# Kernel tuning notes

Hardware: AMD Instinct MI355X
Metric: run time of the kernel (lower is better)

Reference implementation:

```python
import jax, jax.numpy as jnp
import numpy as np

B, T, F_IN, L, D = 512, 32, 4096, 256, 256
EPS = 1e-8
KM_ITERS = 100


def _linear(x, w, b):
    return x @ w.T + b


def _clf(h, w0, b0, w1, b1, w2, b2, w3, b3):
    # Linear->ReLU (Dropout is identity in eval) x3 then final Linear
    h = jax.nn.relu(_linear(h, w0, b0))
    h = jax.nn.relu(_linear(h, w1, b1))
    h = jax.nn.relu(_linear(h, w2, b2))
    return _linear(h, w3, b3)


def _kmeans_cosine(f):
    # f: (T, L). 2-cluster kmeans with cosine distance, fixed iteration count.
    fn = f / (jnp.linalg.norm(f, axis=1, keepdims=True) + EPS)
    centers0 = jnp.stack([f[0], f[T // 2]])  # deterministic init (ref: random pick)

    def step(centers, _):
        cn = centers / (jnp.linalg.norm(centers, axis=1, keepdims=True) + EPS)
        sim = fn @ cn.T                           # (T,2) cosine similarity
        assign = jnp.argmax(sim, axis=1)          # argmin of (1 - sim)
        mask = jax.nn.one_hot(assign, 2, dtype=f.dtype)  # (T,2)
        counts = mask.sum(axis=0)                 # (2,)
        new = (mask.T @ f) / jnp.clip(counts, 1.0)[:, None]
        new = jnp.where(counts[:, None] > 0, new, centers)
        return new, assign

    centers, assigns = jax.lax.scan(step, centers0, None, length=KM_ITERS)
    return assigns[-1], centers


def setup_inputs() -> dict:
    key = jax.random.key(0)
    ks = jax.random.split(key, 32)
    s = 0.02
    inp = {
        "x": jax.random.normal(ks[0], (B, T, F_IN), dtype=jnp.float32),
        "tsn_w": jax.random.normal(ks[1], (L, F_IN, 3), dtype=jnp.float32) * s,
        "tsn_b": jnp.zeros((L,), jnp.float32),
        "aV_w": jax.random.normal(ks[2], (D, L), dtype=jnp.float32) * s,
        "aV_b": jnp.zeros((D,), jnp.float32),
        "aU_w": jax.random.normal(ks[3], (D, L), dtype=jnp.float32) * s,
        "aU_b": jnp.zeros((D,), jnp.float32),
        "gate_w": jax.random.normal(ks[4], (1, D), dtype=jnp.float32) * s,
        "gate_b": jnp.zeros((1,), jnp.float32),
    }
    dims_bag = [(D, L), (D // 2, D), (32, D // 2), (1, 32)]
    dims_seg = [(D, L + 1), (D // 2, D), (32, D // 2), (1, 32)]
    for j, (o, i) in enumerate(dims_bag):
        inp[f"cb_w{j}"] = jax.random.normal(ks[5 + j], (o, i), dtype=jnp.float32) * s
        inp[f"cb_b{j}"] = jnp.zeros((o,), jnp.float32)
    for j, (o, i) in enumerate(dims_seg):
        inp[f"cs_w{j}"] = jax.random.normal(ks[9 + j], (o, i), dtype=jnp.float32) * s
        inp[f"cs_b{j}"] = jnp.zeros((o,), jnp.float32)
    return inp


def reference(x, tsn_w, tsn_b, aV_w, aV_b, aU_w, aU_b, gate_w, gate_b,
              cb_w0, cb_b0, cb_w1, cb_b1, cb_w2, cb_b2, cb_w3, cb_b3,
              cs_w0, cs_b0, cs_w1, cs_b1, cs_w2, cs_b2, cs_w3, cs_b3):
    feat_in = jnp.nan_to_num(x)  # (B,T,4096)
    # Conv1d over time (kernel 3, pad 1): NCH layout
    feature = jax.lax.conv_general_dilated(
        feat_in.transpose(0, 2, 1), tsn_w, (1,), [(1, 1)],
        dimension_numbers=('NCH', 'OIH', 'NCH')) + tsn_b[None, :, None]
    feature = feature.transpose(0, 2, 1)  # (B,T,L)

    # Gated MIL attention
    A_V = jnp.tanh(_linear(feature, aV_w, aV_b))
    A_U = jax.nn.sigmoid(_linear(feature, aU_w, aU_b))
    A = _linear(A_V * A_U, gate_w, gate_b)      # (B,T,1)
    At = A.transpose(0, 2, 1)                   # (B,1,T)
    bag = jnp.einsum('bot,btl->bol', jax.nn.softmax(At, axis=2), feature)[:, 0]  # (B,L)

    output1 = jax.nn.sigmoid(_clf(bag, cb_w0, cb_b0, cb_w1, cb_b1,
                                  cb_w2, cb_b2, cb_w3, cb_b3)).reshape(-1)  # (B,)

    seg_in = jnp.concatenate([feature, A], axis=2)  # (B,T,L+1)
    output_seg = jax.nn.sigmoid(_clf(seg_in, cs_w0, cs_b0, cs_w1, cs_b1,
                                     cs_w2, cs_b2, cs_w3, cs_b3)[..., 0])  # (B,T)

    # Per-sample 2-means cosine clustering (batched via vmap instead of python loop)
    assigns, _ = jax.vmap(_kmeans_cosine)(feature)  # (B,T) int
    mask0 = assigns == 0
    cnt0 = mask0.sum(1).astype(output_seg.dtype)
    cnt1 = T - cnt0
    m0 = jnp.where(mask0, output_seg, 0.0).sum(1) / jnp.clip(cnt0, 1.0)
    m1 = jnp.where(~mask0, output_seg, 0.0).sum(1) / jnp.clip(cnt1, 1.0)
    m0 = jnp.where(cnt0 > 0, m0, -jnp.inf)
    m1 = jnp.where(cnt1 > 0, m1, -jnp.inf)
    output2 = jnp.maximum(m0, m1)  # (B,)

    weight = 0.5
    output = jnp.stack([output1 * weight, output2 * (1.0 - weight)], axis=1)  # (B,2)
    # (ragged cluster index lists replaced by the dense assignment map `assigns`)
    return feature, assigns, output_seg, output, At
```

## Files before the change

### kernel.cpp

```cpp
#include <hip/hip_runtime.h>
#include <cfloat>
#include <cmath>

#define NB 512
#define NT 32
#define FIN 4096
#define NL 256
#define ND 256
#define NM (NB*NT)
#define KCONV (3*FIN)
#define PLANE 3145728

#define BM 128
#define BN 128
#define BK 32
#define LDT 132

typedef __attribute__((ext_vector_type(8))) short short8_t;
typedef __attribute__((ext_vector_type(4))) float f32x4;

__device__ __forceinline__ float sigmoidf_(float v) { return 1.0f / (1.0f + expf(-v)); }

__device__ __forceinline__ unsigned short f2bf(float v) {
  unsigned u = __float_as_uint(v);
  unsigned r = u + 0x7FFFu + ((u >> 16) & 1u);
  return (unsigned short)(r >> 16);
}
__device__ __forceinline__ float bf2f(unsigned short h) {
  return __uint_as_float(((unsigned)h) << 16);
}

__global__ void __launch_bounds__(256) repack_frag_k(const float* __restrict__ w,
                                                     unsigned short* __restrict__ wt) {
  int d = blockIdx.x * 256 + threadIdx.x;
  int kt = d >> 13;
  int bc = (d >> 9) & 15;
  int lane = (d >> 3) & 63;
  int j = d & 7;
  int kb = lane >> 4;
  int kk = kt * 32 + kb * 8 + j;
  int l = bc * 16 + (lane & 15);
  int tap = kk >> 12;
  int f = kk & 4095;
  float v = w[(size_t)l * KCONV + f * 3 + tap];
  unsigned short hi = f2bf(v);
  unsigned short lo = f2bf(v - bf2f(hi));
  wt[d] = hi;
  wt[PLANE + d] = lo;
}

__global__ void __launch_bounds__(256) repack_dense_k(const float* __restrict__ W1,
    const float* __restrict__ W2, int nsplit, int ldw, int KB, int N16,
    unsigned short* __restrict__ wt, int planeElems) {
  int d = blockIdx.x * 256 + threadIdx.x;
  if (d >= planeElems) return;
  int j = d & 7;
  int lane = (d >> 3) & 63;
  int bckt = d >> 9;
  int bc = bckt % N16;
  int kt = bckt / N16;
  int kk = kt * 32 + (lane >> 4) * 8 + j;
  int l = bc * 16 + (lane & 15);
  float v = 0.f;
  if (kk < KB) {
    if (l < nsplit) v = W1[(size_t)l * ldw + kk];
    else            v = W2[(size_t)(l - nsplit) * ldw + kk];
  }
  unsigned short hi = f2bf(v);
  unsigned short lo = f2bf(v - bf2f(hi));
  wt[d] = hi;
  wt[planeElems + d] = lo;
}

__global__ void __launch_bounds__(256) conv_mfma_k(const float* __restrict__ x,
    const unsigned short* __restrict__ WT, float* __restrict__ PART) {
  __shared__ __align__(16) unsigned short AS[8192];
  __shared__ __align__(16) unsigned short BS[8192];
  const int tid = threadIdx.x;
  const int m0 = blockIdx.x * 128;
  const int by = blockIdx.y;
  const int ktBase = blockIdx.z * 192;
  const int lane = tid & 63;
  const int w = tid >> 6, wr = w >> 1, wc = w & 1;
  const int kb = tid & 3;
  const int rquot = tid >> 2;

  f32x4 acc[4][4] = {};
  float4 avreg[4];
  short8_t bvreg[4];

  {
    int ktg = ktBase;
    int tap = ktg >> 7;
    int f0 = (ktg & 127) << 5;
#pragma unroll
    for (int u = 0; u < 2; ++u) {
      int row = u * 64 + rquot;
      int gm = m0 + row;
      int tt = (gm & 31) + tap - 1;
      if ((unsigned)tt < 32u) {
        const float* src = x + (size_t)(gm + tap - 1) * FIN + f0 + kb * 8;
        avreg[u*2+0] = *reinterpret_cast<const float4*>(src);
        avreg[u*2+1] = *reinterpret_cast<const float4*>(src + 4);
      } else {
        avreg[u*2+0] = make_float4(0,0,0,0);
        avreg[u*2+1] = make_float4(0,0,0,0);
      }
    }
    const unsigned short* bsrc = WT + ((size_t)ktg * 16 + by * 8) * 512;
#pragma unroll
    for (int q = 0; q < 4; ++q) {
      int p = q >> 1, pass = q & 1;
      bvreg[q] = *reinterpret_cast<const short8_t*>(bsrc + (size_t)p * PLANE + (pass*256 + tid) * 8);
    }
  }

  for (int i = 0; i < 192; ++i) {
#pragma unroll
    for (int u = 0; u < 2; ++u) {
      float vv[8];
      *reinterpret_cast<float4*>(&vv[0]) = avreg[u*2+0];
      *reinterpret_cast<float4*>(&vv[4]) = avreg[u*2+1];
      __align__(16) unsigned short hi[8];
      __align__(16) unsigned short lo[8];
#pragma unroll
      for (int e = 0; e < 8; ++e) {
        float v = vv[e];
        v = (v == v) ? v : 0.0f;
        unsigned short h = f2bf(v);
        hi[e] = h;
        lo[e] = f2bf(v - bf2f(h));
      }
      int row = u * 64 + rquot;
      int br = row >> 4;
      int lanew = (row & 15) + (kb << 4);
      int off = br * 512 + lanew * 8;
      *reinterpret_cast<short8_t*>(AS + off)        = *reinterpret_cast<const short8_t*>(hi);
      *reinterpret_cast<short8_t*>(AS + 4096 + off) = *reinterpret_cast<const short8_t*>(lo);
    }
#pragma unroll
    for (int q = 0; q < 4; ++q) {
      int p = q >> 1, pass = q & 1;
      *reinterpret_cast<short8_t*>(BS + p * 4096 + (pass*256 + tid) * 8) = bvreg[q];
    }
    __syncthreads();

    if (i + 1 < 192) {
      int ktg = ktBase + i + 1;
      int tap = ktg >> 7;
      int f0 = (ktg & 127) << 5;
#pragma unroll
      for (int u = 0; u < 2; ++u) {
        int row = u * 64 + rquot;
        int gm = m0 + row;
        int tt = (gm & 31) + tap - 1;
        if ((unsigned)tt < 32u) {
          const float* src = x + (size_t)(gm + tap - 1) * FIN + f0 + kb * 8;
          avreg[u*2+0] = *reinterpret_cast<const float4*>(src);
          avreg[u*2+1] = *reinterpret_cast<const float4*>(src + 4);
        } else {
          avreg[u*2+0] = make_float4(0,0,0,0);
          avreg[u*2+1] = make_float4(0,0,0,0);
        }
      }
      const unsigned short* bsrc = WT + ((size_t)ktg * 16 + by * 8) * 512;
#pragma unroll
      for (int q = 0; q < 4; ++q) {
        int p = q >> 1, pass = q & 1;
        bvreg[q] = *reinterpret_cast<const short8_t*>(bsrc + (size_t)p * PLANE + (pass*256 + tid) * 8);
      }
    }

    short8_t bh[4], bl[4];
#pragma unroll
    for (int c = 0; c < 4; ++c) {
      int bc = wc * 4 + c;
      bh[c] = *reinterpret_cast<const short8_t*>(BS + bc * 512 + lane * 8);
      bl[c] = *reinterpret_cast<const short8_t*>(BS + 4096 + bc * 512 + lane * 8);
    }
#pragma unroll
    for (int r = 0; r < 4; ++r) {
      int br = wr * 4 + r;
      short8_t ah = *reinterpret_cast<const short8_t*>(AS + br * 512 + lane * 8);
      short8_t al = *reinterpret_cast<const short8_t*>(AS + 4096 + br * 512 + lane * 8);
#pragma unroll
      for (int c = 0; c < 4; ++c) {
        acc[r][c] = __builtin_amdgcn_mfma_f32_16x16x32_bf16(ah, bh[c], acc[r][c], 0, 0, 0);
        acc[r][c] = __builtin_amdgcn_mfma_f32_16x16x32_bf16(ah, bl[c], acc[r][c], 0, 0, 0);
        acc[r][c] = __builtin_amdgcn_mfma_f32_16x16x32_bf16(al, bh[c], acc[r][c], 0, 0, 0);
      }
    }
    __syncthreads();
  }

  float* P = PART + (size_t)blockIdx.z * ((size_t)NM * NL);
#pragma unroll
  for (int r = 0; r < 4; ++r) {
#pragma unroll
    for (int c = 0; c < 4; ++c) {
#pragma unroll
      for (int e = 0; e < 4; ++e) {
        int row = m0 + wr * 64 + r * 16 + ((lane >> 4) << 2) + e;
        int col = by * 128 + wc * 64 + c * 16 + (lane & 15);
        P[(size_t)row * NL + col] = acc[r][c][e];
      }
    }
  }
}

__global__ void __launch_bounds__(256) reduce_bias_k(const float* __restrict__ PART,
    const float* __restrict__ bias, float* __restrict__ feat) {
  int i = blockIdx.x * 256 + threadIdx.x;
  size_t base = (size_t)i * 4;
  float4 a = *reinterpret_cast<const float4*>(PART + base);
  float4 b = *reinterpret_cast<const float4*>(PART + (size_t)NM * NL + base);
  int c0 = (int)(base & 255);
  float4 bb = *reinterpret_cast<const float4*>(bias + c0);
  float4 o;
  o.x = a.x + b.x + bb.x;
  o.y = a.y + b.y + bb.y;
  o.z = a.z + b.z + bb.z;
  o.w = a.w + b.w + bb.w;
  *reinterpret_cast<float4*>(feat + base) = o;
}

template <int ACT, int SEG>
__global__ void __launch_bounds__(256) mfma_gemm_k(const float* __restrict__ A, int lda,
    const float* __restrict__ Aws, const unsigned short* __restrict__ WT,
    int planeElems, int N16, int KT,
    const float* __restrict__ bias1, const float* __restrict__ bias2, int bsplit,
    float* __restrict__ C, int N) {
  __shared__ __align__(16) unsigned short AS[8192];
  __shared__ __align__(16) unsigned short BS[8192];
  const int tid = threadIdx.x;
  const int m0 = blockIdx.x * 128;
  const int by = blockIdx.y;
  const int lane = tid & 63;
  const int w = tid >> 6, wr = w >> 1, wc = w & 1;
  const int kb = tid & 3;
  const int rquot = tid >> 2;

  f32x4 acc[4][4] = {};
  float4 avreg[4];
  short8_t bvreg[4];

  {
    int kk0 = 0;
#pragma unroll
    for (int u = 0; u < 2; ++u) {
      int gm = m0 + u * 64 + rquot;
      const float* src = A + (size_t)gm * lda + kk0 + kb * 8;
      avreg[u*2+0] = *reinterpret_cast<const float4*>(src);
      avreg[u*2+1] = *reinterpret_cast<const float4*>(src + 4);
    }
    const unsigned short* bsrc = WT + ((size_t)(0 * N16) + by * 8) * 512;
#pragma unroll
    for (int q = 0; q < 4; ++q) {
      int p = q >> 1, pass = q & 1;
      bvreg[q] = *reinterpret_cast<const short8_t*>(bsrc + (size_t)p * planeElems * 8 / 8
                  + (size_t)p * 0 + (pass*256 + tid) * 8 + (size_t)(p ? planeElems - planeElems : 0));
    }
#pragma unroll
    for (int q = 0; q < 4; ++q) {
      int p = q >> 1, pass = q & 1;
      bvreg[q] = *reinterpret_cast<const short8_t*>(WT + (size_t)p * planeElems
                  + ((size_t)by * 8) * 512 + (pass*256 + tid) * 8);
    }
  }

  for (int i = 0; i < KT; ++i) {
#pragma unroll
    for (int u = 0; u < 2; ++u) {
      float vv[8];
      *reinterpret_cast<float4*>(&vv[0]) = avreg[u*2+0];
      *reinterpret_cast<float4*>(&vv[4]) = avreg[u*2+1];
      __align__(16) unsigned short hi[8];
      __align__(16) unsigned short lo[8];
#pragma unroll
      for (int e = 0; e < 8; ++e) {
        float v = vv[e];
        unsigned short h = f2bf(v);
        hi[e] = h;
        lo[e] = f2bf(v - bf2f(h));
      }
      int row = u * 64 + rquot;
      int br = row >> 4;
      int lanew = (row & 15) + (kb << 4);
      int off = br * 512 + lanew * 8;
      *reinterpret_cast<short8_t*>(AS + off)        = *reinterpret_cast<const short8_t*>(hi);
      *reinterpret_cast<short8_t*>(AS + 4096 + off) = *reinterpret_cast<const short8_t*>(lo);
    }
#pragma unroll
    for (int q = 0; q < 4; ++q) {
      int p = q >> 1, pass = q & 1;
      *reinterpret_cast<short8_t*>(BS + p * 4096 + (pass*256 + tid) * 8) = bvreg[q];
    }
    __syncthreads();

    if (i + 1 < KT) {
      int kk0 = (i + 1) * 32;
#pragma unroll
      for (int u = 0; u < 2; ++u) {
        int gm = m0 + u * 64 + rquot;
        if (SEG && kk0 >= 256) {
          float a0 = (kb == 0) ? Aws[gm] : 0.f;
          avreg[u*2+0] = make_float4(a0, 0.f, 0.f, 0.f);
          avreg[u*2+1] = make_float4(0.f, 0.f, 0.f, 0.f);
        } else {
          const float* src = A + (size_t)gm * lda + kk0 + kb * 8;
          avreg[u*2+0] = *reinterpret_cast<const float4*>(src);
          avreg[u*2+1] = *reinterpret_cast<const float4*>(src + 4);
        }
      }
#pragma unroll
      for (int q = 0; q < 4; ++q) {
        int p = q >> 1, pass = q & 1;
        bvreg[q] = *reinterpret_cast<const short8_t*>(WT + (size_t)p * planeElems
                    + ((size_t)(i + 1) * N16 + by * 8) * 512 + (pass*256 + tid) * 8);
      }
    }

    short8_t bh[4], bl[4];
#pragma unroll
    for (int c = 0; c < 4; ++c) {
      int bc = wc * 4 + c;
      bh[c] = *reinterpret_cast<const short8_t*>(BS + bc * 512 + lane * 8);
      bl[c] = *reinterpret_cast<const short8_t*>(BS + 4096 + bc * 512 + lane * 8);
    }
#pragma unroll
    for (int r = 0; r < 4; ++r) {
      int br = wr * 4 + r;
      short8_t ah = *reinterpret_cast<const short8_t*>(AS + br * 512 + lane * 8);
      short8_t al = *reinterpret_cast<const short8_t*>(AS + 4096 + br * 512 + lane * 8);
#pragma unroll
      for (int c = 0; c < 4; ++c) {
        acc[r][c] = __builtin_amdgcn_mfma_f32_16x16x32_bf16(ah, bh[c], acc[r][c], 0, 0, 0);
        acc[r][c] = __builtin_amdgcn_mfma_f32_16x16x32_bf16(ah, bl[c], acc[r][c], 0, 0, 0);
        acc[r][c] = __builtin_amdgcn_mfma_f32_16x16x32_bf16(al, bh[c], acc[r][c], 0, 0, 0);
      }
    }
    __syncthreads();
  }

#pragma unroll
  for (int r = 0; r < 4; ++r) {
#pragma unroll
    for (int c = 0; c < 4; ++c) {
#pragma unroll
      for (int e = 0; e < 4; ++e) {
        int row = m0 + wr * 64 + r * 16 + ((lane >> 4) << 2) + e;
        int col = by * 128 + wc * 64 + c * 16 + (lane & 15);
        float b = (col < bsplit) ? bias1[col] : bias2[col - bsplit];
        float v = acc[r][c][e] + b;
        if (ACT == 1) v = fmaxf(v, 0.f);
        C[(size_t)row * N + col] = v;
      }
    }
  }
}

template <int ACT>
__global__ void __launch_bounds__(256) gemm_wt_k(const float* __restrict__ A, int lda,
    const float* __restrict__ W, int ldw, int KB,
    const float* __restrict__ bias, float* __restrict__ C,
    int N, int K) {
  __shared__ float As[BK][LDT];
  __shared__ float Bs[BK][LDT];
  const int tid = threadIdx.x;
  const int m0 = blockIdx.x * BM;
  const int n0 = blockIdx.y * BN;
  const int row0 = (tid >> 4) << 3;
  const int col0 = (tid & 15) << 3;
  float acc[8][8] = {};
  for (int kk0 = 0; kk0 < K; kk0 += BK) {
#pragma unroll
    for (int i = 0; i < 4; ++i) {
      int v = i * 256 + tid;
      int row = v >> 3;
      int f4 = (v & 7) << 2;
      float4 val = *reinterpret_cast<const float4*>(A + (size_t)(m0 + row) * lda + kk0 + f4);
      As[f4 + 0][row] = val.x;
      As[f4 + 1][row] = val.y;
      As[f4 + 2][row] = val.z;
      As[f4 + 3][row] = val.w;
    }
#pragma unroll
    for (int i = 0; i < 4; ++i) {
      int v = i * 256 + tid;
      int n = v >> 3;
      int kq = (v & 7) << 2;
      int gn = n0 + n;
#pragma unroll
      for (int j = 0; j < 4; ++j) {
        int kk = kk0 + kq + j;
        float bv = 0.f;
        if (gn < N && kk < KB) bv = W[(size_t)gn * ldw + kk];
        Bs[kq + j][n] = bv;
      }
    }
    __syncthreads();
#pragma unroll
    for (int kk = 0; kk < BK; ++kk) {
      float a[8], b[8];
      *reinterpret_cast<float4*>(&a[0]) = *reinterpret_cast<const float4*>(&As[kk][row0]);
      *reinterpret_cast<float4*>(&a[4]) = *reinterpret_cast<const float4*>(&As[kk][row0 + 4]);
      *reinterpret_cast<float4*>(&b[0]) = *reinterpret_cast<const float4*>(&Bs[kk][col0]);
      *reinterpret_cast<float4*>(&b[4]) = *reinterpret_cast<const float4*>(&Bs[kk][col0 + 4]);
#pragma unroll
      for (int r = 0; r < 8; ++r)
#pragma unroll
        for (int c = 0; c < 8; ++c)
          acc[r][c] = fmaf(a[r], b[c], acc[r][c]);
    }
    __syncthreads();
  }
#pragma unroll
  for (int r = 0; r < 8; ++r) {
    int m = m0 + row0 + r;
#pragma unroll
    for (int c = 0; c < 8; ++c) {
      int n = n0 + col0 + c;
      if (n < N) {
        float v = acc[r][c] + bias[n];
        if (ACT == 1) v = fmaxf(v, 0.f);
        C[(size_t)m * (size_t)N + n] = v;
      }
    }
  }
}

__global__ void __launch_bounds__(256) gate_k(const float* __restrict__ Y,
    const float* __restrict__ gw, const float* __restrict__ gb,
    float* __restrict__ Aws, float* __restrict__ At) {
  int lane = threadIdx.x & 63;
  int m = blockIdx.x * 4 + (threadIdx.x >> 6);
  float4 v4 = *reinterpret_cast<const float4*>(Y + (size_t)m * 512 + lane * 4);
  float4 u4 = *reinterpret_cast<const float4*>(Y + (size_t)m * 512 + 256 + lane * 4);
  float4 g4 = *reinterpret_cast<const float4*>(gw + lane * 4);
  float s = tanhf(v4.x) * sigmoidf_(u4.x) * g4.x
          + tanhf(v4.y) * sigmoidf_(u4.y) * g4.y
          + tanhf(v4.z) * sigmoidf_(u4.z) * g4.z
          + tanhf(v4.w) * sigmoidf_(u4.w) * g4.w;
#pragma unroll
  for (int off = 32; off > 0; off >>= 1) s += __shfl_xor(s, off, 64);
  if (lane == 0) {
    float a = s + gb[0];
    Aws[m] = a;
    At[m] = a;
  }
}

__global__ void __launch_bounds__(256) softmax_bag_k(const float* __restrict__ Aws,
    const float* __restrict__ feat, float* __restrict__ bag) {
  __shared__ float av[NT];
  __shared__ float ev[NT];
  int b = blockIdx.x, tid = threadIdx.x;
  if (tid < NT) av[tid] = Aws[b * NT + tid];
  __syncthreads();
  float mx = -FLT_MAX;
#pragma unroll
  for (int t = 0; t < NT; ++t) mx = fmaxf(mx, av[t]);
  if (tid < NT) ev[tid] = expf(av[tid] - mx);
  __syncthreads();
  float ssum = 0.f;
#pragma unroll
  for (int t = 0; t < NT; ++t) ssum += ev[t];
  float accv = 0.f;
#pragma unroll
  for (int t = 0; t < NT; ++t) accv += ev[t] * feat[((size_t)b * NT + t) * NL + tid];
  bag[(size_t)b * NL + tid] = accv / ssum;
}

__global__ void __launch_bounds__(256) rowdot32_k(const float* __restrict__ H,
    const float* __restrict__ w, const float* __restrict__ bptr,
    float* __restrict__ outp, int ostride, float scale) {
  int m = blockIdx.x * 256 + threadIdx.x;
  const float* h = H + (size_t)m * 32;
  float s = bptr[0];
#pragma unroll
  for (int i = 0; i < 32; i += 4) {
    float4 hv = *reinterpret_cast<const float4*>(h + i);
    float4 wv = *reinterpret_cast<const float4*>(w + i);
    s += hv.x * wv.x + hv.y * wv.y + hv.z * wv.z + hv.w * wv.w;
  }
  outp[(size_t)m * ostride] = scale * sigmoidf_(s);
}

__global__ void __launch_bounds__(64) kmeans_k(const float* __restrict__ feat,
    const float* __restrict__ seg, float* __restrict__ assigns_out,
    float* __restrict__ outpair) {
  __shared__ float fls[NT][260];
  int b = blockIdx.x, lane = threadIdx.x;
  int l0 = lane << 2;
  float fn[NT][4];
#pragma unroll
  for (int t = 0; t < NT; ++t) {
    float4 v = *reinterpret_cast<const float4*>(feat + ((size_t)b * NT + t) * NL + l0);
    *reinterpret_cast<float4*>(&fls[t][l0]) = v;
    float ss = v.x * v.x + v.y * v.y + v.z * v.z + v.w * v.w;
#pragma unroll
    for (int off = 32; off > 0; off >>= 1) ss += __shfl_xor(ss, off, 64);
    float nr = sqrtf(ss) + 1e-8f;
    fn[t][0] = v.x / nr; fn[t][1] = v.y / nr; fn[t][2] = v.z / nr; fn[t][3] = v.w / nr;
  }
  __syncthreads();
  float cr0[4], cr1[4];
#pragma unroll
  for (int i = 0; i < 4; ++i) { cr0[i] = fls[0][l0 + i]; cr1[i] = fls[16][l0 + i]; }

  unsigned long long amask = 0ull;
  unsigned long long prev = ~0ull;
  int c1n = 0;
  for (int it = 0; it < 100; ++it) {
    float ss0 = cr0[0]*cr0[0] + cr0[1]*cr0[1] + cr0[2]*cr0[2] + cr0[3]*cr0[3];
    float ss1 = cr1[0]*cr1[0] + cr1[1]*cr1[1] + cr1[2]*cr1[2] + cr1[3]*cr1[3];
#pragma unroll
    for (int off = 32; off > 0; off >>= 1) {
      ss0 += __shfl_xor(ss0, off, 64);
      ss1 += __shfl_xor(ss1, off, 64);
    }
    float nr0 = sqrtf(ss0) + 1e-8f, nr1 = sqrtf(ss1) + 1e-8f;
    float cn0[4], cn1[4];
#pragma unroll
    for (int i = 0; i < 4; ++i) { cn0[i] = cr0[i] / nr0; cn1[i] = cr1[i] / nr1; }
    float p[64];
#pragma unroll
    for (int t = 0; t < NT; ++t) {
      p[2*t]   = fn[t][0]*cn0[0] + fn[t][1]*cn0[1] + fn[t][2]*cn0[2] + fn[t][3]*cn0[3];
      p[2*t+1] = fn[t][0]*cn1[0] + fn[t][1]*cn1[1] + fn[t][2]*cn1[2] + fn[t][3]*cn1[3];
    }
    float v32[32];
    { bool hi = (lane & 32) != 0;
#pragma unroll
      for (int i = 0; i < 32; ++i) {
        float keep = hi ? p[32+i] : p[i];
        float send = hi ? p[i] : p[32+i];
        v32[i] = keep + __shfl_xor(send, 32, 64);
      } }
    float v16[16];
    { bool hi = (lane & 16) != 0;
#pragma unroll
      for (int i = 0; i < 16; ++i) {
        float keep = hi ? v32[16+i] : v32[i];
        float send = hi ? v32[i] : v32[16+i];
        v16[i] = keep + __shfl_xor(send, 16, 64);
      } }
    float v8[8];
    { bool hi = (lane & 8) != 0;
#pragma unroll
      for (int i = 0; i < 8; ++i) {
        float keep = hi ? v16[8+i] : v16[i];
        float send = hi ? v16[i] : v16[8+i];
        v8[i] = keep + __shfl_xor(send, 8, 64);
      } }
    float v4[4];
    { bool hi = (lane & 4) != 0;
#pragma unroll
      for (int i = 0; i < 4; ++i) {
        float keep = hi ? v8[4+i] : v8[i];
        float send = hi ? v8[i] : v8[4+i];
        v4[i] = keep + __shfl_xor(send, 4, 64);
      } }
    float v2[2];
    { bool hi = (lane & 2) != 0;
#pragma unroll
      for (int i = 0; i < 2; ++i) {
        float keep = hi ? v4[2+i] : v4[i];
        float send = hi ? v4[i] : v4[2+i];
        v2[i] = keep + __shfl_xor(send, 2, 64);
      } }
    float sim;
    { bool hi = (lane & 1) != 0;
      float keep = hi ? v2[1] : v2[0];
      float send = hi ? v2[0] : v2[1];
      sim = keep + __shfl_xor(send, 1, 64);
    }
    float simo = __shfl_xor(sim, 1, 64);
    bool is0 = (lane & 1) == 0;
    unsigned long long mask = __ballot(is0 && (simo > sim));
    int c1 = __popcll(mask);
    int c0 = NT - c1;
    amask = mask; c1n = c1;
    if (mask == prev) break;
    prev = mask;
    float s0v[4] = {0,0,0,0}, s1v[4] = {0,0,0,0};
#pragma unroll
    for (int t = 0; t < NT; ++t) {
      float mt = (float)((mask >> (2*t)) & 1ull);
      float nt = 1.0f - mt;
      float4 fv = *reinterpret_cast<const float4*>(&fls[t][l0]);
      s1v[0] = fmaf(mt, fv.x, s1v[0]); s1v[1] = fmaf(mt, fv.y, s1v[1]);
      s1v[2] = fmaf(mt, fv.z, s1v[2]); s1v[3] = fmaf(mt, fv.w, s1v[3]);
      s0v[0] = fmaf(nt, fv.x, s0v[0]); s0v[1] = fmaf(nt, fv.y, s0v[1]);
      s0v[2] = fmaf(nt, fv.z, s0v[2]); s0v[3] = fmaf(nt, fv.w, s0v[3]);
    }
    float fc0 = fmaxf((float)c0, 1.0f), fc1 = fmaxf((float)c1, 1.0f);
#pragma unroll
    for (int i = 0; i < 4; ++i) {
      float n0v = s0v[i] / fc0;
      float n1v = s1v[i] / fc1;
      cr0[i] = (c0 > 0) ? n0v : cr0[i];
      cr1[i] = (c1 > 0) ? n1v : cr1[i];
    }
  }
  if (lane < NT)
    assigns_out[(size_t)b * NT + lane] = (amask & (1ull << (2*lane))) ? 1.0f : 0.0f;
  if (lane == 0) {
    float sum0 = 0.f, sum1 = 0.f;
    for (int t = 0; t < NT; ++t) {
      float sv = seg[(size_t)b * NT + t];
      if (amask & (1ull << (2*t))) sum1 += sv; else sum0 += sv;
    }
    int c1 = c1n, c0 = NT - c1n;
    float m0 = (c0 > 0) ? (sum0 / fmaxf((float)c0, 1.f)) : -INFINITY;
    float m1 = (c1 > 0) ? (sum1 / fmaxf((float)c1, 1.f)) : -INFINITY;
    outpair[(size_t)b * 2 + 1] = 0.5f * fmaxf(m0, m1);
  }
}

extern "C" void kernel_launch(void* const* d_in, const int* in_sizes, int n_in,
                              void* d_out, int out_size, void* d_ws, size_t ws_size,
                              hipStream_t stream) {
  const float* x      = (const float*)d_in[0];
  const float* tsn_w  = (const float*)d_in[1];
  const float* tsn_b  = (const float*)d_in[2];
  const float* aV_w   = (const float*)d_in[3];
  const float* aV_b   = (const float*)d_in[4];
  const float* aU_w   = (const float*)d_in[5];
  const float* aU_b   = (const float*)d_in[6];
  const float* gate_w = (const float*)d_in[7];
  const float* gate_b = (const float*)d_in[8];
  const float* cb_w0  = (const float*)d_in[9];
  const float* cb_b0  = (const float*)d_in[10];
  const float* cb_w1  = (const float*)d_in[11];
  const float* cb_b1  = (const float*)d_in[12];
  const float* cb_w2  = (const float*)d_in[13];
  const float* cb_b2  = (const float*)d_in[14];
  const float* cb_w3  = (const float*)d_in[15];
  const float* cb_b3  = (const float*)d_in[16];
  const float* cs_w0  = (const float*)d_in[17];
  const float* cs_b0  = (const float*)d_in[18];
  const float* cs_w1  = (const float*)d_in[19];
  const float* cs_b1  = (const float*)d_in[20];
  const float* cs_w2  = (const float*)d_in[21];
  const float* cs_b2  = (const float*)d_in[22];
  const float* cs_w3  = (const float*)d_in[23];
  const float* cs_b3  = (const float*)d_in[24];

  float* out = (float*)d_out;
  float* o_feat   = out;
  float* o_assign = out + 4194304;
  float* o_seg    = out + 4210688;
  float* o_out    = out + 4227072;
  float* o_At     = out + 4228096;

  char* ws = (char*)d_ws;
  unsigned short* WT = (unsigned short*)ws;
  float* PART  = (float*)(ws + 12582912);
  unsigned short* WVU = (unsigned short*)ws;
  unsigned short* WC0 = (unsigned short*)(ws + 524288);
  unsigned short* WC1 = (unsigned short*)(ws + 819200);
  float* AWS   = (float*)(ws + 950272);
  float* BAG   = (float*)(ws + 1015808);
  float* BH0   = (float*)(ws + 1540096);
  float* BH1   = (float*)(ws + 2064384);
  float* BH2   = (float*)(ws + 2326528);
  float* Y     = (float*)(ws + 12582912);
  float* SH0   = (float*)(ws + 12582912);
  float* SH1   = (float*)(ws + 29360128);
  float* SH2   = (float*)(ws + 37748736);

  repack_frag_k<<<dim3(12288), dim3(256), 0, stream>>>(tsn_w, WT);
  conv_mfma_k<<<dim3(128, 2, 2), dim3(256), 0, stream>>>(x, WT, PART);
  reduce_bias_k<<<dim3(4096), dim3(256), 0, stream>>>(PART, tsn_b, o_feat);
  repack_dense_k<<<dim3(512), dim3(256), 0, stream>>>(aV_w, aU_w, 256, 256, 256, 32, WVU, 131072);
  repack_dense_k<<<dim3(288), dim3(256), 0, stream>>>(cs_w0, cs_w0, 256, 257, 257, 16, WC0, 73728);
  repack_dense_k<<<dim3(128), dim3(256), 0, stream>>>(cs_w1, cs_w1, 256, 256, 256, 8, WC1, 32768);
  mfma_gemm_k<0,0><<<dim3(128, 4), dim3(256), 0, stream>>>(o_feat, 256, nullptr, WVU,
      131072, 32, 8, aV_b, aU_b, 256, Y, 512);
  gate_k<<<dim3(4096), dim3(256), 0, stream>>>(Y, gate_w, gate_b, AWS, o_At);
  softmax_bag_k<<<dim3(512), dim3(256), 0, stream>>>(AWS, o_feat, BAG);
  gemm_wt_k<1><<<dim3(4, 2), dim3(256), 0, stream>>>(BAG, 256, cb_w0, 256, 256, cb_b0, BH0, 256, 256);
  gemm_wt_k<1><<<dim3(4, 1), dim3(256), 0, stream>>>(BH0, 256, cb_w1, 256, 256, cb_b1, BH1, 128, 256);
  gemm_wt_k<1><<<dim3(4, 1), dim3(256), 0, stream>>>(BH1, 128, cb_w2, 128, 128, cb_b2, BH2, 32, 128);
  rowdot32_k<<<dim3(2), dim3(256), 0, stream>>>(BH2, cb_w3, cb_b3, o_out, 2, 0.5f);
  mfma_gemm_k<1,1><<<dim3(128, 2), dim3(256), 0, stream>>>(o_feat, 256, AWS, WC0,
      73728, 16, 9, cs_b0, cs_b0, 256, SH0, 256);
  mfma_gemm_k<1,0><<<dim3(128, 1), dim3(256), 0, stream>>>(SH0, 256, nullptr, WC1,
      32768, 8, 8, cs_b1, cs_b1, 128, SH1, 128);
  gemm_wt_k<1><<<dim3(128, 1), dim3(256), 0, stream>>>(SH1, 128, cs_w2, 128, 128, cs_b2, SH2, 32, 128);
  rowdot32_k<<<dim3(64), dim3(256), 0, stream>>>(SH2, cs_w3, cs_b3, o_seg, 1, 1.0f);
  kmeans_k<<<dim3(512), dim3(64), 0, stream>>>(o_feat, o_seg, o_assign, o_out);
}
```

Before: 625.6 us.

## Pre-split input to bf16 hi/lo planes and stream conv tiles via async LDS loads

```diff
diff --git a/kernel.cpp b/kernel.cpp
--- a/kernel.cpp
+++ b/kernel.cpp
@@ -10,6 +10,7 @@
 #define NM (NB*NT)
 #define KCONV (3*FIN)
 #define PLANE 3145728
+#define KTILES 192
 
 #define BM 128
 #define BN 128
@@ -28,6 +29,33 @@
 }
 __device__ __forceinline__ float bf2f(unsigned short h) {
   return __uint_as_float(((unsigned)h) << 16);
+}
+
+__global__ void __launch_bounds__(256) xprep_k(const float* __restrict__ x,
+    unsigned short* __restrict__ XPhi, unsigned short* __restrict__ XPlo,
+    unsigned short* __restrict__ ZROW) {
+  size_t i = ((size_t)blockIdx.x * 256 + threadIdx.x) * 8;
+  float4 v0 = *reinterpret_cast<const float4*>(x + i);
+  float4 v1 = *reinterpret_cast<const float4*>(x + i + 4);
+  float vv[8];
+  *reinterpret_cast<float4*>(&vv[0]) = v0;
+  *reinterpret_cast<float4*>(&vv[4]) = v1;
+  __align__(16) unsigned short hi[8];
+  __align__(16) unsigned short lo[8];
+#pragma unroll
+  for (int e = 0; e < 8; ++e) {
+    float v = vv[e];
+    v = (v == v) ? v : 0.0f;
+    unsigned short h = f2bf(v);
+    hi[e] = h;
+    lo[e] = f2bf(v - bf2f(h));
+  }
+  *reinterpret_cast<short8_t*>(XPhi + i) = *reinterpret_cast<const short8_t*>(hi);
+  *reinterpret_cast<short8_t*>(XPlo + i) = *reinterpret_cast<const short8_t*>(lo);
+  if (blockIdx.x == 0 && threadIdx.x < 64) {
+    short8_t z = {0,0,0,0,0,0,0,0};
+    *reinterpret_cast<short8_t*>(ZROW + threadIdx.x * 8) = z;
+  }
 }
 
 __global__ void __launch_bounds__(256) repack_frag_k(const float* __restrict__ w,
@@ -72,6 +100,115 @@
   wt[planeElems + d] = lo;
 }
 
+__global__ void __launch_bounds__(256) conv_mfma2_k(
+    const unsigned short* __restrict__ XPhi, const unsigned short* __restrict__ XPlo,
+    const unsigned short* __restrict__ WT, const unsigned short* __restrict__ ZROW,
+    float* __restrict__ PART) {
+  __shared__ __align__(16) unsigned short LB[2][16384];
+  const int tid = threadIdx.x;
+  const int lane = tid & 63;
+  const int w = tid >> 6;
+  const int wr = w >> 1, wc = w & 1;
+  const int m0 = blockIdx.x * 128;
+  const int by = blockIdx.y;
+  const int ktBase = blockIdx.z * KTILES;
+  const int arow_lo = lane & 15;
+  const int achunk = lane >> 4;
+
+  f32x4 acc[4][4] = {};
+
+  auto stage = [&](int buf, int kt) {
+    const int tap = kt >> 7;
+    const int f0 = (kt & 127) << 5;
+#pragma unroll
+    for (int rb = 0; rb < 2; ++rb) {
+      const int br = (w << 1) + rb;
+      const int gm = m0 + br * 16 + arow_lo;
+      const int tt = (gm & 31) + tap - 1;
+      const unsigned short* sh;
+      const unsigned short* sl;
+      if ((unsigned)tt < 32u) {
+        const size_t off = (size_t)(gm + tap - 1) * 4096 + (size_t)(f0 + (achunk << 3));
+        sh = XPhi + off;
+        sl = XPlo + off;
+      } else {
+        sh = ZROW + (lane << 3);
+        sl = sh;
+      }
+      __builtin_amdgcn_global_load_lds(
+          (const __attribute__((address_space(1))) void*)sh,
+          (__attribute__((address_space(3))) void*)&LB[buf][br << 9], 16, 0, 0);
+      __builtin_amdgcn_global_load_lds(
+          (const __attribute__((address_space(1))) void*)sl,
+          (__attribute__((address_space(3))) void*)&LB[buf][4096 + (br << 9)], 16, 0, 0);
+    }
+#pragma unroll
+    for (int cb = 0; cb < 2; ++cb) {
+      const int bc = (w << 1) + cb;
+      const unsigned short* sh = WT + (((size_t)kt * 16 + (by << 3) + bc) << 9) + (lane << 3);
+      const unsigned short* sl = sh + PLANE;
+      __builtin_amdgcn_global_load_lds(
+          (const __attribute__((address_space(1))) void*)sh,
+          (__attribute__((address_space(3))) void*)&LB[buf][8192 + (bc << 9)], 16, 0, 0);
+      __builtin_amdgcn_global_load_lds(
+          (const __attribute__((address_space(1))) void*)sl,
+          (__attribute__((address_space(3))) void*)&LB[buf][12288 + (bc << 9)], 16, 0, 0);
+    }
+  };
+
+  stage(0, ktBase);
+  for (int i = 0; i < KTILES; ++i) {
+    const int cur = i & 1;
+    if (i + 1 < KTILES) {
+      stage(cur ^ 1, ktBase + i + 1);
+      asm volatile("s_waitcnt vmcnt(8)" ::: "memory");
+    } else {
+      asm volatile("s_waitcnt vmcnt(0)" ::: "memory");
+    }
+    __builtin_amdgcn_sched_barrier(0);
+    __builtin_amdgcn_s_barrier();
+
+    const unsigned short* A0 = &LB[cur][0];
+    const unsigned short* B0 = &LB[cur][8192];
+    short8_t bh[4], bl[4];
+#pragma unroll
+    for (int c = 0; c < 4; ++c) {
+      const int bc = wc * 4 + c;
+      bh[c] = *reinterpret_cast<const short8_t*>(B0 + (bc << 9) + (lane << 3));
+      bl[c] = *reinterpret_cast<const short8_t*>(B0 + 4096 + (bc << 9) + (lane << 3));
+    }
+#pragma unroll
+    for (int r = 0; r < 4; ++r) {
+      const int br = wr * 4 + r;
+      short8_t ah = *reinterpret_cast<const short8_t*>(A0 + (br << 9) + (lane << 3));
+      short8_t al = *reinterpret_cast<const short8_t*>(A0 + 4096 + (br << 9) + (lane << 3));
+#pragma unroll
+      for (int c = 0; c < 4; ++c) {
+        acc[r][c] = __builtin_amdgcn_mfma_f32_16x16x32_bf16(ah, bh[c], acc[r][c], 0, 0, 0);
+        acc[r][c] = __builtin_amdgcn_mfma_f32_16x16x32_bf16(ah, bl[c], acc[r][c], 0, 0, 0);
+        acc[r][c] = __builtin_amdgcn_mfma_f32_16x16x32_bf16(al, bh[c], acc[r][c], 0, 0, 0);
+      }
+    }
+    __builtin_amdgcn_sched_barrier(0);
+    asm volatile("s_waitcnt lgkmcnt(0)" ::: "memory");
+    __builtin_amdgcn_s_barrier();
+  }
+
+  float* P = PART + (size_t)blockIdx.z * ((size_t)NM * NL);
+#pragma unroll
+  for (int r = 0; r < 4; ++r) {
+#pragma unroll
+    for (int c = 0; c < 4; ++c) {
+#pragma unroll
+      for (int e = 0; e < 4; ++e) {
+        int row = m0 + wr * 64 + r * 16 + ((lane >> 4) << 2) + e;
+        int col = by * 128 + wc * 64 + c * 16 + (lane & 15);
+        P[(size_t)row * NL + col] = acc[r][c][e];
+      }
+    }
+  }
+}
+
 __global__ void __launch_bounds__(256) conv_mfma_k(const float* __restrict__ x,
     const unsigned short* __restrict__ WT, float* __restrict__ PART) {
   __shared__ __align__(16) unsigned short AS[8192];
@@ -245,20 +382,12 @@
   short8_t bvreg[4];
 
   {
-    int kk0 = 0;
 #pragma unroll
     for (int u = 0; u < 2; ++u) {
       int gm = m0 + u * 64 + rquot;
-      const float* src = A + (size_t)gm * lda + kk0 + kb * 8;
+      const float* src = A + (size_t)gm * lda + kb * 8;
       avreg[u*2+0] = *reinterpret_cast<const float4*>(src);
       avreg[u*2+1] = *reinterpret_cast<const float4*>(src + 4);
-    }
-    const unsigned short* bsrc = WT + ((size_t)(0 * N16) + by * 8) * 512;
-#pragma unroll
-    for (int q = 0; q < 4; ++q) {
-      int p = q >> 1, pass = q & 1;
-      bvreg[q] = *reinterpret_cast<const short8_t*>(bsrc + (size_t)p * planeElems * 8 / 8
-                  + (size_t)p * 0 + (pass*256 + tid) * 8 + (size_t)(p ? planeElems - planeElems : 0));
     }
 #pragma unroll
     for (int q = 0; q < 4; ++q) {
@@ -669,9 +798,18 @@
   float* SH0   = (float*)(ws + 12582912);
   float* SH1   = (float*)(ws + 29360128);
   float* SH2   = (float*)(ws + 37748736);
+  unsigned short* XPhi = (unsigned short*)(ws + 50331648);
+  unsigned short* XPlo = (unsigned short*)(ws + 184549376);
+  unsigned short* ZROW = (unsigned short*)(ws + 318767104);
+  const bool fast = ws_size >= 318768128ull;
 
   repack_frag_k<<<dim3(12288), dim3(256), 0, stream>>>(tsn_w, WT);
-  conv_mfma_k<<<dim3(128, 2, 2), dim3(256), 0, stream>>>(x, WT, PART);
+  if (fast) {
+    xprep_k<<<dim3(32768), dim3(256), 0, stream>>>(x, XPhi, XPlo, ZROW);
+    conv_mfma2_k<<<dim3(128, 2, 2), dim3(256), 0, stream>>>(XPhi, XPlo, WT, ZROW, PART);
+  } else {
+    conv_mfma_k<<<dim3(128, 2, 2), dim3(256), 0, stream>>>(x, WT, PART);
+  }
   reduce_bias_k<<<dim3(4096), dim3(256), 0, stream>>>(PART, tsn_b, o_feat);
   repack_dense_k<<<dim3(512), dim3(256), 0, stream>>>(aV_w, aU_w, 256, 256, 256, 32, WVU, 131072);
   repack_dense_k<<<dim3(288), dim3(256), 0, stream>>>(cs_w0, cs_w0, 256, 257, 257, 16, WC0, 73728);
```

Measured after the change: 745.3 us. 19.1% more time.

## Double-buffer conv GEMM LDS with direct global-to-LDS B loads and block swizzle

Applied to the files above, without the earlier changes.

```diff
diff --git a/kernel.cpp b/kernel.cpp
--- a/kernel.cpp
+++ b/kernel.cpp
@@ -10,6 +10,7 @@
 #define NM (NB*NT)
 #define KCONV (3*FIN)
 #define PLANE 3145728
+#define KTILES 192
 
 #define BM 128
 #define BN 128
@@ -72,128 +73,130 @@
   wt[planeElems + d] = lo;
 }
 
-__global__ void __launch_bounds__(256) conv_mfma_k(const float* __restrict__ x,
+__global__ void __launch_bounds__(256) conv_mfma3_k(const float* __restrict__ x,
     const unsigned short* __restrict__ WT, float* __restrict__ PART) {
-  __shared__ __align__(16) unsigned short AS[8192];
-  __shared__ __align__(16) unsigned short BS[8192];
+  __shared__ __align__(16) unsigned short LB[2][16384];
   const int tid = threadIdx.x;
-  const int m0 = blockIdx.x * 128;
-  const int by = blockIdx.y;
-  const int ktBase = blockIdx.z * 192;
   const int lane = tid & 63;
-  const int w = tid >> 6, wr = w >> 1, wc = w & 1;
-  const int kb = tid & 3;
-  const int rquot = tid >> 2;
+  const int w = tid >> 6;
+  const int wr = w >> 1, wc = w & 1;
+  const int bid = blockIdx.x;
+  const int swz = ((bid & 7) << 6) + (bid >> 3);
+  const int m0 = (swz & 127) << 7;
+  const int by = (swz >> 7) & 1;
+  const int kz = swz >> 8;
+  const int ktBase = kz * KTILES;
 
   f32x4 acc[4][4] = {};
-  float4 avreg[4];
-  short8_t bvreg[4];
-
-  {
-    int ktg = ktBase;
-    int tap = ktg >> 7;
-    int f0 = (ktg & 127) << 5;
-#pragma unroll
-    for (int u = 0; u < 2; ++u) {
-      int row = u * 64 + rquot;
-      int gm = m0 + row;
-      int tt = (gm & 31) + tap - 1;
+  float4 avA[4];
+
+  auto loadA = [&](int kt, float4* av) {
+#pragma unroll
+    for (int rb = 0; rb < 2; ++rb) {
+      const int br = (w << 1) + rb;
+      const int gm = m0 + br * 16 + (lane & 15);
+      const int tap = kt >> 7;
+      const int f0 = (kt & 127) << 5;
+      const int tt = (gm & 31) + tap - 1;
       if ((unsigned)tt < 32u) {
-        const float* src = x + (size_t)(gm + tap - 1) * FIN + f0 + kb * 8;
-        avreg[u*2+0] = *reinterpret_cast<const float4*>(src);
-        avreg[u*2+1] = *reinterpret_cast<const float4*>(src + 4);
+        const float* src = x + (size_t)(gm + tap - 1) * FIN + f0 + ((lane >> 4) << 3);
+        av[rb*2+0] = *reinterpret_cast<const float4*>(src);
+        av[rb*2+1] = *reinterpret_cast<const float4*>(src + 4);
       } else {
-        avreg[u*2+0] = make_float4(0,0,0,0);
-        avreg[u*2+1] = make_float4(0,0,0,0);
-      }
-    }
-    const unsigned short* bsrc = WT + ((size_t)ktg * 16 + by * 8) * 512;
-#pragma unroll
-    for (int q = 0; q < 4; ++q) {
-      int p = q >> 1, pass = q & 1;
-      bvreg[q] = *reinterpret_cast<const short8_t*>(bsrc + (size_t)p * PLANE + (pass*256 + tid) * 8);
-    }
-  }
-
-  for (int i = 0; i < 192; ++i) {
-#pragma unroll
-    for (int u = 0; u < 2; ++u) {
+        av[rb*2+0] = make_float4(0.f,0.f,0.f,0.f);
+        av[rb*2+1] = make_float4(0.f,0.f,0.f,0.f);
+      }
+    }
+  };
+  auto writeA = [&](int buf, const float4* av) {
+#pragma unroll
+    for (int rb = 0; rb < 2; ++rb) {
       float vv[8];
-      *reinterpret_cast<float4*>(&vv[0]) = avreg[u*2+0];
-      *reinterpret_cast<float4*>(&vv[4]) = avreg[u*2+1];
-      __align__(16) unsigned short hi[8];
-      __align__(16) unsigned short lo[8];
+      *reinterpret_cast<float4*>(&vv[0]) = av[rb*2+0];
+      *reinterpret_cast<float4*>(&vv[4]) = av[rb*2+1];
+      __align__(16) unsigned short hi8[8];
+      __align__(16) unsigned short lo8[8];
 #pragma unroll
       for (int e = 0; e < 8; ++e) {
         float v = vv[e];
         v = (v == v) ? v : 0.0f;
         unsigned short h = f2bf(v);
-        hi[e] = h;
-        lo[e] = f2bf(v - bf2f(h));
-      }
-      int row = u * 64 + rquot;
-      int br = row >> 4;
-      int lanew = (row & 15) + (kb << 4);
-      int off = br * 512 + lanew * 8;
-      *reinterpret_cast<short8_t*>(AS + off)        = *reinterpret_cast<const short8_t*>(hi);
-      *reinterpret_cast<short8_t*>(AS + 4096 + off) = *reinterpret_cast<const short8_t*>(lo);
-    }
-#pragma unroll
-    for (int q = 0; q < 4; ++q) {
-      int p = q >> 1, pass = q & 1;
-      *reinterpret_cast<short8_t*>(BS + p * 4096 + (pass*256 + tid) * 8) = bvreg[q];
-    }
-    __syncthreads();
-
-    if (i + 1 < 192) {
-      int ktg = ktBase + i + 1;
-      int tap = ktg >> 7;
-      int f0 = (ktg & 127) << 5;
-#pragma unroll
-      for (int u = 0; u < 2; ++u) {
-        int row = u * 64 + rquot;
-        int gm = m0 + row;
-        int tt = (gm & 31) + tap - 1;
-        if ((unsigned)tt < 32u) {
-          const float* src = x + (size_t)(gm + tap - 1) * FIN + f0 + kb * 8;
-          avreg[u*2+0] = *reinterpret_cast<const float4*>(src);
-          avreg[u*2+1] = *reinterpret_cast<const float4*>(src + 4);
-        } else {
-          avreg[u*2+0] = make_float4(0,0,0,0);
-          avreg[u*2+1] = make_float4(0,0,0,0);
+        hi8[e] = h;
+        lo8[e] = f2bf(v - bf2f(h));
+      }
+      const int br = (w << 1) + rb;
+      const int off = (br << 9) + (lane << 3);
+      *reinterpret_cast<short8_t*>(&LB[buf][off])        = *reinterpret_cast<const short8_t*>(hi8);
+      *reinterpret_cast<short8_t*>(&LB[buf][4096 + off]) = *reinterpret_cast<const short8_t*>(lo8);
+    }
+  };
+  auto stageB = [&](int buf, int kt) {
+#pragma unroll
+    for (int cb = 0; cb < 2; ++cb) {
+      const int bc = (w << 1) + cb;
+      const unsigned short* sh = WT + (((size_t)kt * 16 + (by << 3) + bc) << 9) + (lane << 3);
+      __builtin_amdgcn_global_load_lds(
+          (const __attribute__((address_space(1))) void*)sh,
+          (__attribute__((address_space(3))) void*)&LB[buf][8192 + (bc << 9)], 16, 0, 0);
+      __builtin_amdgcn_global_load_lds(
+          (const __attribute__((address_space(1))) void*)(sh + PLANE),
+          (__attribute__((address_space(3))) void*)&LB[buf][12288 + (bc << 9)], 16, 0, 0);
+    }
+  };
+
+  stageB(0, ktBase);
+  loadA(ktBase, avA);
+  asm volatile("s_waitcnt vmcnt(0)" ::: "memory");
+  writeA(0, avA);
+  loadA(ktBase + 1, avA);
+  stageB(1, ktBase + 1);
+  asm volatile("s_waitcnt lgkmcnt(0)" ::: "memory");
+  __builtin_amdgcn_s_barrier();
+
+  for (int i = 0; i < KTILES; ++i) {
+    const int cur = i & 1;
+    if (i + 1 < KTILES) {
+      asm volatile("s_waitcnt vmcnt(4)" ::: "memory");
+      writeA(cur ^ 1, avA);
+      if (i + 2 < KTILES) loadA(ktBase + i + 2, avA);
+    }
+    {
+      const unsigned short* A0 = &LB[cur][0];
+      const unsigned short* B0 = &LB[cur][8192];
+      short8_t bh[4], bl[4];
+#pragma unroll
+      for (int c = 0; c < 4; ++c) {
+        const int bc = wc * 4 + c;
+        bh[c] = *reinterpret_cast<const short8_t*>(B0 + (bc << 9) + (lane << 3));
+        bl[c] = *reinterpret_cast<const short8_t*>(B0 + 4096 + (bc << 9) + (lane << 3));
+      }
+#pragma unroll
+      for (int r = 0; r < 4; ++r) {
+        const int br = wr * 4 + r;
+        short8_t ah = *reinterpret_cast<const short8_t*>(A0 + (br << 9) + (lane << 3));
+        short8_t al = *reinterpret_cast<const short8_t*>(A0 + 4096 + (br << 9) + (lane << 3));
+#pragma unroll
+        for (int c = 0; c < 4; ++c) {
+          acc[r][c] = __builtin_amdgcn_mfma_f32_16x16x32_bf16(ah, bh[c], acc[r][c], 0, 0, 0);
+          acc[r][c] = __builtin_amdgcn_mfma_f32_16x16x32_bf16(ah, bl[c], acc[r][c], 0, 0, 0);
+          acc[r][c] = __builtin_amdgcn_mfma_f32_16x16x32_bf16(al, bh[c], acc[r][c], 0, 0, 0);
         }
       }
-      const unsigned short* bsrc = WT + ((size_t)ktg * 16 + by * 8) * 512;
-#pragma unroll
-      for (int q = 0; q < 4; ++q) {
-        int p = q >> 1, pass = q & 1;
-        bvreg[q] = *reinterpret_cast<const short8_t*>(bsrc + (size_t)p * PLANE + (pass*256 + tid) * 8);
-      }
-    }
-
-    short8_t bh[4], bl[4];
-#pragma unroll
-    for (int c = 0; c < 4; ++c) {
-      int bc = wc * 4 + c;
-      bh[c] = *reinterpret_cast<const short8_t*>(BS + bc * 512 + lane * 8);
-      bl[c] = *reinterpret_cast<const short8_t*>(BS + 4096 + bc * 512 + lane * 8);
-    }
-#pragma unroll
-    for (int r = 0; r < 4; ++r) {
-      int br = wr * 4 + r;
-      short8_t ah = *reinterpret_cast<const short8_t*>(AS + br * 512 + lane * 8);
-      short8_t al = *reinterpret_cast<const short8_t*>(AS + 4096 + br * 512 + lane * 8);
-#pragma unroll
-      for (int c = 0; c < 4; ++c) {
-        acc[r][c] = __builtin_amdgcn_mfma_f32_16x16x32_bf16(ah, bh[c], acc[r][c], 0, 0, 0);
-        acc[r][c] = __builtin_amdgcn_mfma_f32_16x16x32_bf16(ah, bl[c], acc[r][c], 0, 0, 0);
-        acc[r][c] = __builtin_amdgcn_mfma_f32_16x16x32_bf16(al, bh[c], acc[r][c], 0, 0, 0);
-      }
-    }
-    __syncthreads();
-  }
-
-  float* P = PART + (size_t)blockIdx.z * ((size_t)NM * NL);
+    }
+    if (i + 1 < KTILES) {
+      if (i + 2 < KTILES) {
+        asm volatile("s_waitcnt vmcnt(4)" ::: "memory");
+      } else {
+        asm volatile("s_waitcnt vmcnt(0)" ::: "memory");
+      }
+      asm volatile("s_waitcnt lgkmcnt(0)" ::: "memory");
+      __builtin_amdgcn_sched_barrier(0);
+      __builtin_amdgcn_s_barrier();
+      if (i + 2 < KTILES) stageB(cur, ktBase + i + 2);
+    }
+  }
+
+  float* P = PART + (size_t)kz * ((size_t)NM * NL);
 #pragma unroll
   for (int r = 0; r < 4; ++r) {
 #pragma unroll
@@ -245,20 +248,12 @@
   short8_t bvreg[4];
 
   {
-    int kk0 = 0;
 #pragma unroll
     for (int u = 0; u < 2; ++u) {
       int gm = m0 + u * 64 + rquot;
-      const float* src = A + (size_t)gm * lda + kk0 + kb * 8;
+      const float* src = A + (size_t)gm * lda + kb * 8;
       avreg[u*2+0] = *reinterpret_cast<const float4*>(src);
       avreg[u*2+1] = *reinterpret_cast<const float4*>(src + 4);
-    }
-    const unsigned short* bsrc = WT + ((size_t)(0 * N16) + by * 8) * 512;
-#pragma unroll
-    for (int q = 0; q < 4; ++q) {
-      int p = q >> 1, pass = q & 1;
-      bvreg[q] = *reinterpret_cast<const short8_t*>(bsrc + (size_t)p * planeElems * 8 / 8
-                  + (size_t)p * 0 + (pass*256 + tid) * 8 + (size_t)(p ? planeElems - planeElems : 0));
     }
 #pragma unroll
     for (int q = 0; q < 4; ++q) {
@@ -671,7 +666,7 @@
   float* SH2   = (float*)(ws + 37748736);
 
   repack_frag_k<<<dim3(12288), dim3(256), 0, stream>>>(tsn_w, WT);
-  conv_mfma_k<<<dim3(128, 2, 2), dim3(256), 0, stream>>>(x, WT, PART);
+  conv_mfma3_k<<<dim3(512), dim3(256), 0, stream>>>(x, WT, PART);
   reduce_bias_k<<<dim3(4096), dim3(256), 0, stream>>>(PART, tsn_b, o_feat);
   repack_dense_k<<<dim3(512), dim3(256), 0, stream>>>(aV_w, aU_w, 256, 256, 256, 32, WVU, 131072);
   repack_dense_k<<<dim3(288), dim3(256), 0, stream>>>(cs_w0, cs_w0, 256, 257, 257, 16, WC0, 73728);
```

Result: slower. 736.1 us (+17.6%).
